# Kernel tuning notes

Measured on AMD Instinct MI355X. Metric: run time of the kernel, lower is better.

The kernel has to match this reference:

```python
import jax, jax.numpy as jnp
import numpy as np
import math

INPUT_SIZE = 1024
HIDDEN_SIZE = 1024
BATCH = 4096


def setup_inputs() -> dict:
    key = jax.random.key(0)
    ks = jax.random.split(key, 16)
    stddev = 1.0 / math.sqrt(HIDDEN_SIZE)

    def unif(k, shape):
        return jax.random.uniform(k, shape, minval=-stddev, maxval=stddev, dtype=jnp.float32)

    inp = {
        'x': jax.random.normal(ks[0], (BATCH, INPUT_SIZE), dtype=jnp.float32),
        'h_prev': jax.random.normal(ks[1], (BATCH, HIDDEN_SIZE), dtype=jnp.float32),
        'c_prev': jax.random.normal(ks[2], (BATCH, HIDDEN_SIZE), dtype=jnp.float32),
        'igx': unif(ks[3], (INPUT_SIZE, HIDDEN_SIZE)),
        'igu': unif(ks[4], (HIDDEN_SIZE, HIDDEN_SIZE)),
        'ib': unif(ks[5], (HIDDEN_SIZE,)),
        'fgx': unif(ks[6], (INPUT_SIZE, HIDDEN_SIZE)),
        'fgu': unif(ks[7], (HIDDEN_SIZE, HIDDEN_SIZE)),
        'fb': unif(ks[8], (HIDDEN_SIZE,)),
        'ogx': unif(ks[9], (INPUT_SIZE, HIDDEN_SIZE)),
        'ogu': unif(ks[10], (HIDDEN_SIZE, HIDDEN_SIZE)),
        'ob': unif(ks[11], (HIDDEN_SIZE,)),
        'cgx': unif(ks[12], (INPUT_SIZE, HIDDEN_SIZE)),
        'cgu': unif(ks[13], (HIDDEN_SIZE, HIDDEN_SIZE)),
        'cb': unif(ks[14], (HIDDEN_SIZE,)),
    }
    return inp


def reference(x, h_prev, c_prev, igx, igu, ib, fgx, fgu, fb, ogx, ogu, ob, cgx, cgu, cb):
    # Fuse the 8 gate matmuls into 2 GEMMs via concatenated weights.
    # Wx: [input_size, 4H], Wh: [hidden, 4H], b: [4H]; gate order i,f,o,c.
    Wx = jnp.concatenate([igx, fgx, ogx, cgx], axis=1)
    Wh = jnp.concatenate([igu, fgu, ogu, cgu], axis=1)
    b = jnp.concatenate([ib, fb, ob, cb], axis=0)
    gates = x @ Wx + h_prev @ Wh + b  # [B, 4H]
    H = c_prev.shape[-1]
    ig = jax.nn.sigmoid(gates[:, 0 * H:1 * H])
    fg = jax.nn.sigmoid(gates[:, 1 * H:2 * H])
    og = jax.nn.sigmoid(gates[:, 2 * H:3 * H])
    cc = jnp.tanh(gates[:, 3 * H:4 * H])
    c = fg * c_prev + ig * cc
    h = og * jnp.tanh(c)
    return (h, c)
```

## Files before the change

kernel.cpp:

```cpp
#include <hip/hip_runtime.h>
#include <hip/hip_bf16.h>

typedef unsigned short u16;
typedef unsigned int u32;
typedef short bf16x8 __attribute__((ext_vector_type(8)));
typedef float f32x4 __attribute__((ext_vector_type(4)));
typedef u16 u16x8 __attribute__((ext_vector_type(8)));

#define HID 1024
#define BATCH 4096
#define KTOT 2048

__device__ __forceinline__ u16 f2bf(float f) {
  u32 v = __builtin_bit_cast(u32, f);
  u32 r = (v + 0x7fffu + ((v >> 16) & 1u)) >> 16;
  return (u16)r;
}
__device__ __forceinline__ float sigmoid_fast(float x) {
  return 1.0f / (1.0f + __expf(-x));
}
__device__ __forceinline__ float tanh_fast(float x) {
  return 2.0f * sigmoid_fast(2.0f * x) - 1.0f;
}
__device__ __forceinline__ void gl_lds16(const void* g, void* l) {
  __builtin_amdgcn_global_load_lds(
      (const __attribute__((address_space(1))) u32*)g,
      (__attribute__((address_space(3))) u32*)l, 16, 0, 0);
}

__global__ __launch_bounds__(256) void prep_xh(
    const float* __restrict__ x, const float* __restrict__ hp,
    u16* __restrict__ xh) {
  int c = blockIdx.x * 256 + threadIdx.x;
  int row = c >> 8;
  int col0 = (c & 255) << 3;
  const float* src = (col0 < 1024) ? (x + (size_t)row * 1024 + col0)
                                   : (hp + (size_t)row * 1024 + (col0 - 1024));
  f32x4 a = *(const f32x4*)(src);
  f32x4 b = *(const f32x4*)(src + 4);
  u16x8 v;
#pragma unroll
  for (int j = 0; j < 4; ++j) { v[j] = f2bf(a[j]); v[j + 4] = f2bf(b[j]); }
  *(u16x8*)(xh + (size_t)row * KTOT + col0) = v;
}

__global__ __launch_bounds__(256) void prep_w(
    const float* __restrict__ igx, const float* __restrict__ fgx,
    const float* __restrict__ ogx, const float* __restrict__ cgx,
    const float* __restrict__ igu, const float* __restrict__ fgu,
    const float* __restrict__ ogu, const float* __restrict__ cgu,
    u16* __restrict__ bt) {
  __shared__ u16 lds[64 * 66];
  const float* srcs[8] = {igx, fgx, ogx, cgx, igu, fgu, ogu, cgu};
  int bid = blockIdx.x;
  int m = bid >> 8;
  int tile = bid & 255;
  int th = tile & 15, tk = tile >> 4;
  int h0 = th << 6, k0 = tk << 6;
  int g = m & 3, which = m >> 2;
  const float* W = srcs[m] + (size_t)k0 * HID + h0;

  int t = threadIdx.x;

  int r1 = t >> 4;
  int c1 = (t & 15) << 2;
#pragma unroll
  for (int p = 0; p < 4; ++p) {
    int row = (p << 4) + r1;
    f32x4 v = *(const f32x4*)(W + (size_t)row * HID + c1);
    u32 p0 = (u32)f2bf(v[0]) | ((u32)f2bf(v[1]) << 16);
    u32 p1 = (u32)f2bf(v[2]) | ((u32)f2bf(v[3]) << 16);
    u32* d = (u32*)&lds[row * 66 + c1];
    d[0] = p0;
    d[1] = p1;
  }
  __syncthreads();

  int nl = t >> 2;
  int kc = t & 3;
  int row_np = ((h0 >> 4) << 6) + ((nl >> 4) << 6) + (g << 4) + (nl & 15);
  size_t dst = (size_t)row_np * KTOT + (size_t)which * 1024 + k0;
  u16x8 a, b;
#pragma unroll
  for (int j = 0; j < 8; ++j) {
    a[j] = lds[(kc * 8 + j) * 66 + nl];
    b[j] = lds[(kc * 8 + 32 + j) * 66 + nl];
  }
  *(u16x8*)(&bt[dst + kc * 8]) = a;
  *(u16x8*)(&bt[dst + kc * 8 + 32]) = b;
}

__global__ __launch_bounds__(256) void lstm_gemm(
    const u16* __restrict__ xh, const u16* __restrict__ bt,
    const float* __restrict__ cprev,
    const float* __restrict__ ib, const float* __restrict__ fb,
    const float* __restrict__ ob, const float* __restrict__ cb,
    float* __restrict__ hout, float* __restrict__ cout) {
  __shared__ u16 As[2 * 128 * 32];
  __shared__ u16 Bs[2 * 128 * 32];

  int t = threadIdx.x;
  int brow = blockIdx.x, bcol = blockIdx.y;
  int w = t >> 6, l = t & 63;
  int wr = (w >> 1) * 64, wc = (w & 1) * 64;
  int lrow = l & 15, quad = l >> 4;

  f32x4 acc[4][4] = {};

  int srow = t >> 2;
  int schunk = ((t & 3) ^ ((t >> 3) & 3)) << 3;
  int quadp = ((quad ^ ((lrow >> 1) & 3)) << 3);
  int grow = brow * 128;
  size_t brow_b = (size_t)(bcol * 128);

  const u16* arow0 = xh + (size_t)(grow + srow) * KTOT + schunk;
  const u16* arow1 = xh + (size_t)(grow + srow + 64) * KTOT + schunk;
  const u16* brow0 = bt + (brow_b + srow) * KTOT + schunk;
  const u16* brow1 = bt + (brow_b + srow + 64) * KTOT + schunk;

  for (int kt = 0; kt < 32; ++kt) {
    __syncthreads();
    int kk = kt * 64;
    gl_lds16(arow0 + kk, &As[t * 8]);
    gl_lds16(arow1 + kk, &As[(t + 256) * 8]);
    gl_lds16(arow0 + kk + 32, &As[4096 + t * 8]);
    gl_lds16(arow1 + kk + 32, &As[4096 + (t + 256) * 8]);
    gl_lds16(brow0 + kk, &Bs[t * 8]);
    gl_lds16(brow1 + kk, &Bs[(t + 256) * 8]);
    gl_lds16(brow0 + kk + 32, &Bs[4096 + t * 8]);
    gl_lds16(brow1 + kk + 32, &Bs[4096 + (t + 256) * 8]);
    __syncthreads();

#pragma unroll
    for (int s = 0; s < 2; ++s) {
      int base = s * 4096;
      bf16x8 af[4], bfr[4];
#pragma unroll
      for (int i = 0; i < 4; ++i) {
        af[i]  = *(const bf16x8*)&As[base + (wr + i * 16 + lrow) * 32 + quadp];
        bfr[i] = *(const bf16x8*)&Bs[base + (wc + i * 16 + lrow) * 32 + quadp];
      }
#pragma unroll
      for (int mi = 0; mi < 4; ++mi)
#pragma unroll
        for (int ni = 0; ni < 4; ++ni)
          acc[mi][ni] = __builtin_amdgcn_mfma_f32_16x16x32_bf16(
              af[mi], bfr[ni], acc[mi][ni], 0, 0, 0);
    }
  }

  int sb = bcol * 2 + (w & 1);
  int hcol = sb * 16 + lrow;
  float bi = ib[hcol];
  float bff = fb[hcol];
  float bo = ob[hcol];
  float bc = cb[hcol];

#pragma unroll
  for (int mi = 0; mi < 4; ++mi) {
    int row0 = grow + wr + mi * 16 + quad * 4;
#pragma unroll
    for (int r = 0; r < 4; ++r) {
      size_t idx = (size_t)(row0 + r) * HID + hcol;
      float gi = sigmoid_fast(acc[mi][0][r] + bi);
      float gf = sigmoid_fast(acc[mi][1][r] + bff);
      float go = sigmoid_fast(acc[mi][2][r] + bo);
      float gc = tanh_fast(acc[mi][3][r] + bc);
      float cp = cprev[idx];
      float cv = gf * cp + gi * gc;
      float hv = go * tanh_fast(cv);
      hout[idx] = hv;
      cout[idx] = cv;
    }
  }
}

extern "C" void kernel_launch(void* const* d_in, const int* in_sizes, int n_in,
                              void* d_out, int out_size, void* d_ws, size_t ws_size,
                              hipStream_t stream) {
  const float* x   = (const float*)d_in[0];
  const float* hp  = (const float*)d_in[1];
  const float* cp  = (const float*)d_in[2];
  const float* igx = (const float*)d_in[3];
  const float* igu = (const float*)d_in[4];
  const float* ib  = (const float*)d_in[5];
  const float* fgx = (const float*)d_in[6];
  const float* fgu = (const float*)d_in[7];
  const float* fb  = (const float*)d_in[8];
  const float* ogx = (const float*)d_in[9];
  const float* ogu = (const float*)d_in[10];
  const float* ob  = (const float*)d_in[11];
  const float* cgx = (const float*)d_in[12];
  const float* cgu = (const float*)d_in[13];
  const float* cb  = (const float*)d_in[14];

  u16* bt = (u16*)d_ws;
  u16* xh = bt + (size_t)4096 * 2048;
  float* hout = (float*)d_out;
  float* cout = hout + (size_t)BATCH * HID;

  prep_xh<<<4096, 256, 0, stream>>>(x, hp, xh);
  prep_w<<<2048, 256, 0, stream>>>(igx, fgx, ogx, cgx, igu, fgu, ogu, cgu, bt);
  lstm_gemm<<<dim3(32, 32), 256, 0, stream>>>(xh, bt, cp, ib, fb, ob, cb,
                                              hout, cout);
}
```

Measured before the change: 220.0 us.

## Enlarge GEMM tiles to 256x256 with multi-stage async LDS pipeline and fuse prep kernels

The two prep kernels are merged into a single launch that branches on block index, saving one launch. The GEMM moves from 128x128 tiles with 256 threads to 256x256 tiles with 512 threads (8 waves of 128x64 each). It also adds a deeper software pipeline: global-to-LDS loads are issued several stages ahead with vmcnt waits, double-buffered 64-wide K tiles, per-phase barriers and MFMA priority boosts. This is meant to raise operand reuse and overlap memory with MFMA. In exchange it needs more LDS and registers per block, and the grid shrinks to 256 blocks, which may leave some of the many CUs with uneven load.

```diff
diff --git a/kernel.cpp b/kernel.cpp
--- a/kernel.cpp
+++ b/kernel.cpp
@@ -10,6 +10,8 @@
 #define HID 1024
 #define BATCH 4096
 #define KTOT 2048
+#define NT 32
+#define LDS_OP 16384
 
 __device__ __forceinline__ u16 f2bf(float f) {
   u32 v = __builtin_bit_cast(u32, f);
@@ -28,31 +30,31 @@
       (__attribute__((address_space(3))) u32*)l, 16, 0, 0);
 }
 
-__global__ __launch_bounds__(256) void prep_xh(
+__global__ __launch_bounds__(256) void prep_all(
     const float* __restrict__ x, const float* __restrict__ hp,
-    u16* __restrict__ xh) {
-  int c = blockIdx.x * 256 + threadIdx.x;
-  int row = c >> 8;
-  int col0 = (c & 255) << 3;
-  const float* src = (col0 < 1024) ? (x + (size_t)row * 1024 + col0)
-                                   : (hp + (size_t)row * 1024 + (col0 - 1024));
-  f32x4 a = *(const f32x4*)(src);
-  f32x4 b = *(const f32x4*)(src + 4);
-  u16x8 v;
-#pragma unroll
-  for (int j = 0; j < 4; ++j) { v[j] = f2bf(a[j]); v[j + 4] = f2bf(b[j]); }
-  *(u16x8*)(xh + (size_t)row * KTOT + col0) = v;
-}
-
-__global__ __launch_bounds__(256) void prep_w(
     const float* __restrict__ igx, const float* __restrict__ fgx,
     const float* __restrict__ ogx, const float* __restrict__ cgx,
     const float* __restrict__ igu, const float* __restrict__ fgu,
     const float* __restrict__ ogu, const float* __restrict__ cgu,
-    u16* __restrict__ bt) {
+    u16* __restrict__ xh, u16* __restrict__ bt) {
   __shared__ u16 lds[64 * 66];
+  if (blockIdx.x < 4096) {
+    int c = blockIdx.x * 256 + threadIdx.x;
+    int row = c >> 8;
+    int col0 = (c & 255) << 3;
+    const float* src = (col0 < 1024)
+                           ? (x + (size_t)row * 1024 + col0)
+                           : (hp + (size_t)row * 1024 + (col0 - 1024));
+    f32x4 a = *(const f32x4*)(src);
+    f32x4 b = *(const f32x4*)(src + 4);
+    u16x8 v;
+#pragma unroll
+    for (int j = 0; j < 4; ++j) { v[j] = f2bf(a[j]); v[j + 4] = f2bf(b[j]); }
+    *(u16x8*)(xh + (size_t)row * KTOT + col0) = v;
+    return;
+  }
   const float* srcs[8] = {igx, fgx, ogx, cgx, igu, fgu, ogu, cgu};
-  int bid = blockIdx.x;
+  int bid = blockIdx.x - 4096;
   int m = bid >> 8;
   int tile = bid & 255;
   int th = tile & 15, tk = tile >> 4;
@@ -61,7 +63,6 @@
   const float* W = srcs[m] + (size_t)k0 * HID + h0;
 
   int t = threadIdx.x;
-
   int r1 = t >> 4;
   int c1 = (t & 15) << 2;
 #pragma unroll
@@ -75,101 +76,142 @@
     d[1] = p1;
   }
   __syncthreads();
-
   int nl = t >> 2;
   int kc = t & 3;
   int row_np = ((h0 >> 4) << 6) + ((nl >> 4) << 6) + (g << 4) + (nl & 15);
   size_t dst = (size_t)row_np * KTOT + (size_t)which * 1024 + k0;
-  u16x8 a, b;
+  u16x8 a2, b2;
 #pragma unroll
   for (int j = 0; j < 8; ++j) {
-    a[j] = lds[(kc * 8 + j) * 66 + nl];
-    b[j] = lds[(kc * 8 + 32 + j) * 66 + nl];
-  }
-  *(u16x8*)(&bt[dst + kc * 8]) = a;
-  *(u16x8*)(&bt[dst + kc * 8 + 32]) = b;
-}
-
-__global__ __launch_bounds__(256) void lstm_gemm(
+    a2[j] = lds[(kc * 8 + j) * 66 + nl];
+    b2[j] = lds[(kc * 8 + 32 + j) * 66 + nl];
+  }
+  *(u16x8*)(&bt[dst + kc * 8]) = a2;
+  *(u16x8*)(&bt[dst + kc * 8 + 32]) = b2;
+}
+
+__device__ __forceinline__ void stage(int s, const u16* aS, const u16* bS,
+                                      u16* lds, int sx) {
+  if (s >= 4 * NT) return;
+  int ts = s >> 2, hh = s & 3;
+  int op = (hh >> 1) ^ 1;
+  int rb = (hh & 1) << 7;
+  const u16* src = (op ? bS : aS) + (size_t)rb * KTOT + ts * 64;
+  u16* dst = lds + ((((ts & 1) << 1) + op) * LDS_OP) + (rb << 6) + sx * 8;
+  gl_lds16(src, dst);
+  gl_lds16(src + (size_t)64 * KTOT, dst + 4096);
+}
+
+__global__ __launch_bounds__(512, 2) void lstm_gemm(
     const u16* __restrict__ xh, const u16* __restrict__ bt,
     const float* __restrict__ cprev,
     const float* __restrict__ ib, const float* __restrict__ fb,
     const float* __restrict__ ob, const float* __restrict__ cb,
     float* __restrict__ hout, float* __restrict__ cout) {
-  __shared__ u16 As[2 * 128 * 32];
-  __shared__ u16 Bs[2 * 128 * 32];
-
-  int t = threadIdx.x;
+  __shared__ __align__(16) u16 lds[2 * 2 * LDS_OP];
+
+  int sx = threadIdx.x;
   int brow = blockIdx.x, bcol = blockIdx.y;
-  int w = t >> 6, l = t & 63;
-  int wr = (w >> 1) * 64, wc = (w & 1) * 64;
-  int lrow = l & 15, quad = l >> 4;
-
-  f32x4 acc[4][4] = {};
-
-  int srow = t >> 2;
-  int schunk = ((t & 3) ^ ((t >> 3) & 3)) << 3;
-  int quadp = ((quad ^ ((lrow >> 1) & 3)) << 3);
-  int grow = brow * 128;
-  size_t brow_b = (size_t)(bcol * 128);
-
-  const u16* arow0 = xh + (size_t)(grow + srow) * KTOT + schunk;
-  const u16* arow1 = xh + (size_t)(grow + srow + 64) * KTOT + schunk;
-  const u16* brow0 = bt + (brow_b + srow) * KTOT + schunk;
-  const u16* brow1 = bt + (brow_b + srow + 64) * KTOT + schunk;
-
-  for (int kt = 0; kt < 32; ++kt) {
-    __syncthreads();
-    int kk = kt * 64;
-    gl_lds16(arow0 + kk, &As[t * 8]);
-    gl_lds16(arow1 + kk, &As[(t + 256) * 8]);
-    gl_lds16(arow0 + kk + 32, &As[4096 + t * 8]);
-    gl_lds16(arow1 + kk + 32, &As[4096 + (t + 256) * 8]);
-    gl_lds16(brow0 + kk, &Bs[t * 8]);
-    gl_lds16(brow1 + kk, &Bs[(t + 256) * 8]);
-    gl_lds16(brow0 + kk + 32, &Bs[4096 + t * 8]);
-    gl_lds16(brow1 + kk + 32, &Bs[4096 + (t + 256) * 8]);
-    __syncthreads();
-
-#pragma unroll
-    for (int s = 0; s < 2; ++s) {
-      int base = s * 4096;
-      bf16x8 af[4], bfr[4];
-#pragma unroll
-      for (int i = 0; i < 4; ++i) {
-        af[i]  = *(const bf16x8*)&As[base + (wr + i * 16 + lrow) * 32 + quadp];
-        bfr[i] = *(const bf16x8*)&Bs[base + (wc + i * 16 + lrow) * 32 + quadp];
-      }
-#pragma unroll
-      for (int mi = 0; mi < 4; ++mi)
-#pragma unroll
-        for (int ni = 0; ni < 4; ++ni)
-          acc[mi][ni] = __builtin_amdgcn_mfma_f32_16x16x32_bf16(
-              af[mi], bfr[ni], acc[mi][ni], 0, 0, 0);
-    }
-  }
-
-  int sb = bcol * 2 + (w & 1);
-  int hcol = sb * 16 + lrow;
+  int w = sx >> 6, l = sx & 63;
+  int wr = (w >> 2) << 7;
+  int wc = (w & 3) << 6;
+  int lrow = l & 15, q = l >> 4;
+  int grow = brow << 8;
+
+  int prow = sx >> 3;
+  int koff = ((sx & 7) ^ (prow & 7)) << 3;
+  const u16* aSrc = xh + (size_t)(grow + prow) * KTOT + koff;
+  const u16* bSrc = bt + (size_t)(bcol * 256 + prow) * KTOT + koff;
+
+  int aoff = (wr + lrow) << 6;
+  int boff = (wc + lrow) << 6;
+  int pc0 = (q ^ (lrow & 7)) << 3;
+  int pc1 = ((q + 4) ^ (lrow & 7)) << 3;
+
+  f32x4 acc[8][4] = {};
+  bf16x8 af[2][2], bfr[4][2];
+
+  stage(0, aSrc, bSrc, lds, sx);
+  stage(1, aSrc, bSrc, lds, sx);
+  stage(2, aSrc, bSrc, lds, sx);
+  stage(3, aSrc, bSrc, lds, sx);
+  stage(4, aSrc, bSrc, lds, sx);
+  asm volatile("s_waitcnt vmcnt(2)");
+  __builtin_amdgcn_s_barrier();
+  __builtin_amdgcn_sched_barrier(0);
+
+#define RDA(i, s) (*(const bf16x8*)(Ab + aoff + (i) * 1024 + ((s) ? pc1 : pc0)))
+#define RDB(j, s) (*(const bf16x8*)(Bb + boff + (j) * 1024 + ((s) ? pc1 : pc0)))
+
+#define DO_PHASE(K_, SS_)                                                     \
+  {                                                                           \
+    af[0][0] = RDA(2 * (K_), 0);                                              \
+    af[0][1] = RDA(2 * (K_), 1);                                              \
+    af[1][0] = RDA(2 * (K_) + 1, 0);                                          \
+    af[1][1] = RDA(2 * (K_) + 1, 1);                                          \
+    if ((K_) == 0) {                                                          \
+      bfr[0][0] = RDB(0, 0); bfr[0][1] = RDB(0, 1);                           \
+      bfr[1][0] = RDB(1, 0); bfr[1][1] = RDB(1, 1);                           \
+      bfr[2][0] = RDB(2, 0); bfr[2][1] = RDB(2, 1);                           \
+      bfr[3][0] = RDB(3, 0); bfr[3][1] = RDB(3, 1);                           \
+    }                                                                         \
+    stage(SS_, aSrc, bSrc, lds, sx);                                          \
+    __builtin_amdgcn_s_barrier();                                             \
+    asm volatile("s_waitcnt lgkmcnt(0)");                                     \
+    __builtin_amdgcn_sched_barrier(0);                                        \
+    __builtin_amdgcn_s_setprio(1);                                            \
+    _Pragma("unroll") for (int s2 = 0; s2 < 2; ++s2) {                        \
+      _Pragma("unroll") for (int j = 0; j < 4; ++j) {                         \
+        acc[2 * (K_)][j] = __builtin_amdgcn_mfma_f32_16x16x32_bf16(           \
+            af[0][s2], bfr[j][s2], acc[2 * (K_)][j], 0, 0, 0);                \
+        acc[2 * (K_) + 1][j] = __builtin_amdgcn_mfma_f32_16x16x32_bf16(       \
+            af[1][s2], bfr[j][s2], acc[2 * (K_) + 1][j], 0, 0, 0);            \
+      }                                                                       \
+    }                                                                         \
+    __builtin_amdgcn_s_setprio(0);                                            \
+    __builtin_amdgcn_sched_barrier(0);                                        \
+  }
+
+#pragma unroll 2
+  for (int t = 0; t < NT; ++t) {
+    const u16* Ab = lds + ((t & 1) << 1) * LDS_OP;
+    const u16* Bb = Ab + LDS_OP;
+    int s0 = 4 * t + 5;
+    DO_PHASE(0, s0)
+    __builtin_amdgcn_s_barrier();
+    DO_PHASE(1, s0 + 1)
+    __builtin_amdgcn_s_barrier();
+    DO_PHASE(2, s0 + 2)
+    __builtin_amdgcn_s_barrier();
+    DO_PHASE(3, s0 + 3)
+    if (t < NT - 2) asm volatile("s_waitcnt vmcnt(2)");
+    else            asm volatile("s_waitcnt vmcnt(0)");
+    __builtin_amdgcn_s_barrier();
+  }
+#undef DO_PHASE
+#undef RDA
+#undef RDB
+
+  int sb = (bcol << 2) + (w & 3);
+  int hcol = (sb << 4) + lrow;
   float bi = ib[hcol];
   float bff = fb[hcol];
   float bo = ob[hcol];
   float bc = cb[hcol];
 
 #pragma unroll
-  for (int mi = 0; mi < 4; ++mi) {
-    int row0 = grow + wr + mi * 16 + quad * 4;
+  for (int i = 0; i < 8; ++i) {
+    int row0 = grow + wr + i * 16 + q * 4;
 #pragma unroll
     for (int r = 0; r < 4; ++r) {
       size_t idx = (size_t)(row0 + r) * HID + hcol;
-      float gi = sigmoid_fast(acc[mi][0][r] + bi);
-      float gf = sigmoid_fast(acc[mi][1][r] + bff);
-      float go = sigmoid_fast(acc[mi][2][r] + bo);
-      float gc = tanh_fast(acc[mi][3][r] + bc);
+      float gi = sigmoid_fast(acc[i][0][r] + bi);
+      float gf = sigmoid_fast(acc[i][1][r] + bff);
+      float go = sigmoid_fast(acc[i][2][r] + bo);
+      float gc = tanh_fast(acc[i][3][r] + bc);
       float cp = cprev[idx];
       float cv = gf * cp + gi * gc;
-      float hv = go * tanh_fast(cv);
-      hout[idx] = hv;
+      hout[idx] = go * tanh_fast(cv);
       cout[idx] = cv;
     }
   }
@@ -199,8 +241,8 @@
   float* hout = (float*)d_out;
   float* cout = hout + (size_t)BATCH * HID;
 
-  prep_xh<<<4096, 256, 0, stream>>>(x, hp, xh);
-  prep_w<<<2048, 256, 0, stream>>>(igx, fgx, ogx, cgx, igu, fgu, ogu, cgu, bt);
-  lstm_gemm<<<dim3(32, 32), 256, 0, stream>>>(xh, bt, cp, ib, fb, ob, cb,
+  prep_all<<<6144, 256, 0, stream>>>(x, hp, igx, fgx, ogx, cgx,
+                                     igu, fgu, ogu, cgu, xh, bt);
+  lstm_gemm<<<dim3(16, 16), 512, 0, stream>>>(xh, bt, cp, ib, fb, ob, cb,
                                               hout, cout);
 }
```

New measurement: 203.5 us. -7.5%, faster.
